# Kernel tuning notes

Measured on AMD Instinct MI355X. Metric: run time of the kernel, lower is better.

Reference implementation:

```python
import jax, jax.numpy as jnp
import numpy as np

B, S, D, H = 4, 2048, 768, 3072

def _layernorm(X):
    # manual LayerNorm: biased variance, no eps, no affine
    mu = jnp.mean(X, axis=2, keepdims=True)
    sigma = jnp.sqrt(jnp.mean(jnp.square(X - mu), axis=2, keepdims=True))
    return (X - mu) / sigma

def setup_inputs() -> dict:
    key = jax.random.key(0)
    ks = jax.random.split(key, 11)
    sc = 0.02
    return {
        "X": jax.random.normal(ks[0], (B, S, D), dtype=jnp.float32),
        "Wq": jax.random.normal(ks[1], (D, D), dtype=jnp.float32) * sc,
        "bq": jnp.zeros((D,), dtype=jnp.float32),
        "Wk": jax.random.normal(ks[2], (D, D), dtype=jnp.float32) * sc,
        "bk": jnp.zeros((D,), dtype=jnp.float32),
        "Wv": jax.random.normal(ks[3], (D, D), dtype=jnp.float32) * sc,
        "bv": jnp.zeros((D,), dtype=jnp.float32),
        "W1": jax.random.normal(ks[4], (D, H), dtype=jnp.float32) * sc,
        "b1": jnp.zeros((H,), dtype=jnp.float32),
        "W2": jax.random.normal(ks[5], (H, D), dtype=jnp.float32) * sc,
        "b2": jnp.zeros((D,), dtype=jnp.float32),
    }

def reference(X, Wq, bq, Wk, bk, Wv, bv, W1, b1, W2, b2):
    dk = jnp.sqrt(jnp.asarray(X.shape[2], dtype=X.dtype))
    Q = X @ Wq + bq
    K = X @ Wk + bk
    V = X @ Wv + bv
    A = jnp.einsum('bqd,bkd->bqk', Q, K)
    # faithful: tril zeroes (not -inf) above-diagonal BEFORE softmax
    A = jnp.tril(A) / dk
    A = jax.nn.softmax(A, axis=2)
    # faithful to einsum 'ijk,ijl->ijl': sum A over k, broadcast onto V
    AV = jnp.sum(A, axis=2, keepdims=True) * V
    X = _layernorm(X + AV)
    F = jax.nn.relu(X @ W1 + b1) @ W2 + b2
    X = _layernorm(X + F)
    return X
```

## Files before the change

kernel.cpp:

```cpp
#include <hip/hip_runtime.h>
#include <hip/hip_bf16.h>
#include <math.h>


typedef __bf16 bf16x8 __attribute__((ext_vector_type(8)));
typedef float f32x4 __attribute__((ext_vector_type(4)));

__device__ inline void gload_lds16(const __hip_bfloat16* g, void* lds) {
  __builtin_amdgcn_global_load_lds(
      (const __attribute__((address_space(1))) void*)g,
      (__attribute__((address_space(3))) void*)lds, 16, 0, 0);
}

__device__ inline float bf2f(unsigned short u) {
  union { unsigned int i; float f; } x;
  x.i = ((unsigned int)u) << 16;
  return x.f;
}

#define BARRIER() asm volatile("s_barrier" ::: "memory")

template <int BNv, int EPI>
__global__ __launch_bounds__(256, 2) void gemm128(
    const __hip_bfloat16* __restrict__ A, const __hip_bfloat16* __restrict__ Bt,
    __hip_bfloat16* __restrict__ C, const float* __restrict__ bias,
    const float* __restrict__ residf, const __hip_bfloat16* __restrict__ residb,
    int M, int N, int K) {
  constexpr int NF = BNv / 32;
  constexpr int BI = BNv / 32;
  constexpr int BS = BNv * 128;
  constexpr int S = 4 + BI;
  __shared__ __align__(16) char smem[32768 + 2 * BS];

  const int bid = blockIdx.x;
  const int mB = M / 128;
  const int rowBase = (bid % mB) * 128;
  const int colBase = (bid / mB) * BNv;
  const int nt = K / 64;

  const int wv = threadIdx.x >> 6;
  const int lane = threadIdx.x & 63;
  const int wr = wv >> 1, wc = wv & 1;
  const int l16 = lane & 15, lk = lane >> 4;

  const int rA = lane >> 3;
  const int cSw = ((lane & 7) ^ rA) * 8;
  const __hip_bfloat16* gA = A + (size_t)(rowBase + wv * 32 + rA) * K + cSw;
  const __hip_bfloat16* gB =
      Bt + (size_t)(colBase + wv * 8 * BI + rA) * K + cSw;

  auto STAGE = [&](int kt, int b) {
    const size_t ko = (size_t)kt * 64;
#pragma unroll
    for (int i = 0; i < 4; ++i)
      gload_lds16(gA + (size_t)i * 8 * K + ko,
                  smem + b * 16384 + (wv * 4 + i) * 1024);
#pragma unroll
    for (int i = 0; i < BI; ++i)
      gload_lds16(gB + (size_t)i * 8 * K + ko,
                  smem + 32768 + b * BS + (wv * BI + i) * 1024);
  };

  const int aBase = (wr * 64 + l16) * 128;
  const int bBase = (wc * (BNv / 2) + l16) * 128;
  const int xr = l16 & 7;
  const int cph0 = ((lk) ^ xr) * 16;
  const int cph1 = ((4 + lk) ^ xr) * 16;

  f32x4 acc[4][NF];
#pragma unroll
  for (int m = 0; m < 4; ++m)
#pragma unroll
    for (int n = 0; n < NF; ++n) acc[m][n] = (f32x4){0.f, 0.f, 0.f, 0.f};

  STAGE(0, 0);
  if (nt > 1) {
    STAGE(1, 1);
    if constexpr (BNv == 128)
      asm volatile("s_waitcnt vmcnt(8)" ::: "memory");
    else
      asm volatile("s_waitcnt vmcnt(7)" ::: "memory");
  } else {
    asm volatile("s_waitcnt vmcnt(0)" ::: "memory");
  }
  BARRIER();

  for (int t = 0; t < nt; ++t) {
    const int b = t & 1;
    const char* pa = smem + b * 16384 + aBase;
    const char* pb = smem + 32768 + b * BS + bBase;

    bf16x8 af0[4], af1[4], bf0[NF], bf1[NF];
#pragma unroll
    for (int m = 0; m < 4; ++m) af0[m] = *(const bf16x8*)(pa + m * 2048 + cph0);
#pragma unroll
    for (int n = 0; n < NF; ++n) bf0[n] = *(const bf16x8*)(pb + n * 2048 + cph0);
#pragma unroll
    for (int m = 0; m < 4; ++m) af1[m] = *(const bf16x8*)(pa + m * 2048 + cph1);
#pragma unroll
    for (int n = 0; n < NF; ++n) bf1[n] = *(const bf16x8*)(pb + n * 2048 + cph1);

    if constexpr (NF == 4)
      asm volatile("s_waitcnt lgkmcnt(8)" ::: "memory");
    else
      asm volatile("s_waitcnt lgkmcnt(7)" ::: "memory");
    __builtin_amdgcn_sched_barrier(0);
    __builtin_amdgcn_s_setprio(1);
#pragma unroll
    for (int m = 0; m < 4; ++m)
#pragma unroll
      for (int n = 0; n < NF; ++n)
        acc[m][n] = __builtin_amdgcn_mfma_f32_16x16x32_bf16(af0[m], bf0[n],
                                                            acc[m][n], 0, 0, 0);
    __builtin_amdgcn_s_setprio(0);
    asm volatile("s_waitcnt lgkmcnt(0)" ::: "memory");
    __builtin_amdgcn_sched_barrier(0);
    __builtin_amdgcn_s_setprio(1);
#pragma unroll
    for (int m = 0; m < 4; ++m)
#pragma unroll
      for (int n = 0; n < NF; ++n)
        acc[m][n] = __builtin_amdgcn_mfma_f32_16x16x32_bf16(af1[m], bf1[n],
                                                            acc[m][n], 0, 0, 0);
    __builtin_amdgcn_s_setprio(0);

    BARRIER();
    if (t + 2 < nt) {
      STAGE(t + 2, b);
      if constexpr (BNv == 128)
        asm volatile("s_waitcnt vmcnt(8)" ::: "memory");
      else
        asm volatile("s_waitcnt vmcnt(7)" ::: "memory");
      BARRIER();
    } else if (t + 2 == nt) {
      asm volatile("s_waitcnt vmcnt(0)" ::: "memory");
      BARRIER();
    }
  }

#pragma unroll
  for (int m = 0; m < 4; ++m) {
#pragma unroll
    for (int n = 0; n < NF; ++n) {
#pragma unroll
      for (int j = 0; j < 4; ++j) {
        const int r = rowBase + wr * 64 + m * 16 + lk * 4 + j;
        const int c = colBase + wc * (BNv / 2) + n * 16 + l16;
        const size_t idx = (size_t)r * N + c;
        float v = acc[m][n][j] + bias[c];
        if (EPI == 1) v += residf[idx];
        if (EPI == 2) v = fmaxf(v, 0.f);
        if (EPI == 3) v += __bfloat162float(residb[idx]);
        C[idx] = __float2bfloat16(v);
      }
    }
  }
}

template <bool OUTF>
__global__ __launch_bounds__(256) void ln_simple(
    const __hip_bfloat16* __restrict__ Y, __hip_bfloat16* __restrict__ outb,
    float* __restrict__ outf) {
  const int wave = threadIdx.x >> 6, lane = threadIdx.x & 63;
  const size_t base = ((size_t)blockIdx.x * 4 + wave) * 768;

  float v[12];
  float s = 0.f, q = 0.f;
#pragma unroll
  for (int c = 0; c < 3; ++c) {
    const int col = c * 256 + lane * 4;
    ushort4 a = *reinterpret_cast<const ushort4*>(&Y[base + col]);
    float y0 = bf2f(a.x), y1 = bf2f(a.y), y2 = bf2f(a.z), y3 = bf2f(a.w);
    v[c * 4 + 0] = y0; v[c * 4 + 1] = y1; v[c * 4 + 2] = y2; v[c * 4 + 3] = y3;
    s += y0 + y1 + y2 + y3;
    q += y0 * y0 + y1 * y1 + y2 * y2 + y3 * y3;
  }
#pragma unroll
  for (int off = 32; off; off >>= 1) {
    s += __shfl_xor(s, off);
    q += __shfl_xor(q, off);
  }
  const float mu = s * (1.f / 768.f);
  const float rs = rsqrtf(q * (1.f / 768.f) - mu * mu);
#pragma unroll
  for (int c = 0; c < 3; ++c) {
    const int col = c * 256 + lane * 4;
    if (OUTF) {
      float4 o;
      o.x = (v[c * 4 + 0] - mu) * rs;
      o.y = (v[c * 4 + 1] - mu) * rs;
      o.z = (v[c * 4 + 2] - mu) * rs;
      o.w = (v[c * 4 + 3] - mu) * rs;
      *reinterpret_cast<float4*>(&outf[base + col]) = o;
    } else {
      __hip_bfloat16 h0 = __float2bfloat16((v[c * 4 + 0] - mu) * rs);
      __hip_bfloat16 h1 = __float2bfloat16((v[c * 4 + 1] - mu) * rs);
      __hip_bfloat16 h2 = __float2bfloat16((v[c * 4 + 2] - mu) * rs);
      __hip_bfloat16 h3 = __float2bfloat16((v[c * 4 + 3] - mu) * rs);
      ushort4 o;
      o.x = *reinterpret_cast<unsigned short*>(&h0);
      o.y = *reinterpret_cast<unsigned short*>(&h1);
      o.z = *reinterpret_cast<unsigned short*>(&h2);
      o.w = *reinterpret_cast<unsigned short*>(&h3);
      *reinterpret_cast<ushort4*>(&outb[base + col]) = o;
    }
  }
}

__global__ __launch_bounds__(256) void cast_bf16_kernel(
    const float* __restrict__ in, __hip_bfloat16* __restrict__ out, int n4) {
  int i = blockIdx.x * blockDim.x + threadIdx.x;
  if (i >= n4) return;
  float4 v = reinterpret_cast<const float4*>(in)[i];
  __hip_bfloat16 h0 = __float2bfloat16(v.x), h1 = __float2bfloat16(v.y);
  __hip_bfloat16 h2 = __float2bfloat16(v.z), h3 = __float2bfloat16(v.w);
  ushort4 o;
  o.x = *reinterpret_cast<unsigned short*>(&h0);
  o.y = *reinterpret_cast<unsigned short*>(&h1);
  o.z = *reinterpret_cast<unsigned short*>(&h2);
  o.w = *reinterpret_cast<unsigned short*>(&h3);
  reinterpret_cast<ushort4*>(out)[i] = o;
}

__global__ __launch_bounds__(256) void transpose_cast(
    const float* __restrict__ W, __hip_bfloat16* __restrict__ Wt, int K, int N) {
  __shared__ float tile[32][33];
  const int t = threadIdx.x;
  const int tx = t & 31;
  const int ty = t >> 5;
  const int n0 = blockIdx.x * 32;
  const int k0 = blockIdx.y * 32;
#pragma unroll
  for (int i = 0; i < 32; i += 8)
    tile[ty + i][tx] = W[(size_t)(k0 + ty + i) * N + n0 + tx];
  __syncthreads();
#pragma unroll
  for (int i = 0; i < 32; i += 8)
    Wt[(size_t)(n0 + ty + i) * K + k0 + tx] = __float2bfloat16(tile[tx][ty + i]);
}

extern "C" void kernel_launch(void* const* d_in, const int* in_sizes, int n_in,
                              void* d_out, int out_size, void* d_ws,
                              size_t ws_size, hipStream_t stream) {
  const float* X = (const float*)d_in[0];
  const float* Wv = (const float*)d_in[5];
  const float* bv = (const float*)d_in[6];
  const float* W1 = (const float*)d_in[7];
  const float* b1 = (const float*)d_in[8];
  const float* W2 = (const float*)d_in[9];
  const float* b2 = (const float*)d_in[10];
  float* out = (float*)d_out;

  const int M = 4 * 2048;
  const int D = 768, H = 3072;

  char* ws = (char*)d_ws;
  __hip_bfloat16* Xb  = (__hip_bfloat16*)(ws);
  __hip_bfloat16* Wvt = (__hip_bfloat16*)(ws + 12582912);
  __hip_bfloat16* W1t = (__hip_bfloat16*)(ws + 13762560);
  __hip_bfloat16* W2t = (__hip_bfloat16*)(ws + 18481152);
  __hip_bfloat16* Yb  = (__hip_bfloat16*)(ws + 23199744);
  __hip_bfloat16* X1b = (__hip_bfloat16*)(ws + 35782656);
  __hip_bfloat16* Gb  = (__hip_bfloat16*)(ws + 48365568);
  __hip_bfloat16* Y2b = Yb;

  cast_bf16_kernel<<<dim3((M * D / 4 + 255) / 256), 256, 0, stream>>>(X, Xb,
                                                                      M * D / 4);
  transpose_cast<<<dim3(D / 32, D / 32), 256, 0, stream>>>(Wv, Wvt, D, D);
  transpose_cast<<<dim3(H / 32, D / 32), 256, 0, stream>>>(W1, W1t, D, H);
  transpose_cast<<<dim3(D / 32, H / 32), 256, 0, stream>>>(W2, W2t, H, D);

  gemm128<96, 1><<<512, 256, 0, stream>>>(Xb, Wvt, Yb, bv, X, nullptr, M, D, D);
  ln_simple<false><<<M / 4, 256, 0, stream>>>(Yb, X1b, nullptr);
  gemm128<128, 2><<<1536, 256, 0, stream>>>(X1b, W1t, Gb, b1, nullptr, nullptr,
                                            M, H, D);
  gemm128<96, 3><<<512, 256, 0, stream>>>(Gb, W2t, Y2b, b2, nullptr, X1b, M, D,
                                          H);
  ln_simple<true><<<M / 4, 256, 0, stream>>>(Y2b, nullptr, out);
}
```

Before: 130.1 us.

## Issue next-stage prefetch mid-iteration and merge prep kernels into one launch

Inside the GEMM main loop, the barrier and the global-to-LDS STAGE load for tile t+2 are moved ahead of the second MFMA half. This lets the prefetch overlap with compute and removes one barrier per iteration. The four preprocessing kernels (X cast and three weight transpose-casts) are merged into a single kernel indexed by block ID, cutting launch overhead. The earlier STAGE may overwrite an LDS buffer while the second MFMA half still reads its fragments; this is only safe if those fragments are already in registers, which the lgkmcnt(0) wait before the barrier appears to ensure.

```diff
diff --git a/kernel.cpp b/kernel.cpp
--- a/kernel.cpp
+++ b/kernel.cpp
@@ -29,7 +29,6 @@
   constexpr int NF = BNv / 32;
   constexpr int BI = BNv / 32;
   constexpr int BS = BNv * 128;
-  constexpr int S = 4 + BI;
   __shared__ __align__(16) char smem[32768 + 2 * BS];
 
   const int bid = blockIdx.x;
@@ -115,6 +114,10 @@
     __builtin_amdgcn_s_setprio(0);
     asm volatile("s_waitcnt lgkmcnt(0)" ::: "memory");
     __builtin_amdgcn_sched_barrier(0);
+    BARRIER();
+
+    if (t + 2 < nt) STAGE(t + 2, b);
+
     __builtin_amdgcn_s_setprio(1);
 #pragma unroll
     for (int m = 0; m < 4; ++m)
@@ -124,16 +127,15 @@
                                                             acc[m][n], 0, 0, 0);
     __builtin_amdgcn_s_setprio(0);
 
-    BARRIER();
-    if (t + 2 < nt) {
-      STAGE(t + 2, b);
-      if constexpr (BNv == 128)
-        asm volatile("s_waitcnt vmcnt(8)" ::: "memory");
-      else
-        asm volatile("s_waitcnt vmcnt(7)" ::: "memory");
-      BARRIER();
-    } else if (t + 2 == nt) {
-      asm volatile("s_waitcnt vmcnt(0)" ::: "memory");
+    if (t + 1 < nt) {
+      if (t + 2 < nt) {
+        if constexpr (BNv == 128)
+          asm volatile("s_waitcnt vmcnt(8)" ::: "memory");
+        else
+          asm volatile("s_waitcnt vmcnt(7)" ::: "memory");
+      } else {
+        asm volatile("s_waitcnt vmcnt(0)" ::: "memory");
+      }
       BARRIER();
     }
   }
@@ -207,29 +209,12 @@
   }
 }
 
-__global__ __launch_bounds__(256) void cast_bf16_kernel(
-    const float* __restrict__ in, __hip_bfloat16* __restrict__ out, int n4) {
-  int i = blockIdx.x * blockDim.x + threadIdx.x;
-  if (i >= n4) return;
-  float4 v = reinterpret_cast<const float4*>(in)[i];
-  __hip_bfloat16 h0 = __float2bfloat16(v.x), h1 = __float2bfloat16(v.y);
-  __hip_bfloat16 h2 = __float2bfloat16(v.z), h3 = __float2bfloat16(v.w);
-  ushort4 o;
-  o.x = *reinterpret_cast<unsigned short*>(&h0);
-  o.y = *reinterpret_cast<unsigned short*>(&h1);
-  o.z = *reinterpret_cast<unsigned short*>(&h2);
-  o.w = *reinterpret_cast<unsigned short*>(&h3);
-  reinterpret_cast<ushort4*>(out)[i] = o;
-}
-
-__global__ __launch_bounds__(256) void transpose_cast(
-    const float* __restrict__ W, __hip_bfloat16* __restrict__ Wt, int K, int N) {
+__device__ inline void tc_tile(const float* __restrict__ W,
+                               __hip_bfloat16* __restrict__ Wt, int K, int N,
+                               int n0, int k0, int t) {
   __shared__ float tile[32][33];
-  const int t = threadIdx.x;
   const int tx = t & 31;
   const int ty = t >> 5;
-  const int n0 = blockIdx.x * 32;
-  const int k0 = blockIdx.y * 32;
 #pragma unroll
   for (int i = 0; i < 32; i += 8)
     tile[ty + i][tx] = W[(size_t)(k0 + ty + i) * N + n0 + tx];
@@ -237,6 +222,36 @@
 #pragma unroll
   for (int i = 0; i < 32; i += 8)
     Wt[(size_t)(n0 + ty + i) * K + k0 + tx] = __float2bfloat16(tile[tx][ty + i]);
+}
+
+__global__ __launch_bounds__(256) void prep_kernel(
+    const float* __restrict__ X, const float* __restrict__ Wv,
+    const float* __restrict__ W1, const float* __restrict__ W2,
+    __hip_bfloat16* __restrict__ Xb, __hip_bfloat16* __restrict__ Wvt,
+    __hip_bfloat16* __restrict__ W1t, __hip_bfloat16* __restrict__ W2t) {
+  const int bid = blockIdx.x;
+  const int t = threadIdx.x;
+  if (bid < 6144) {
+    const int i = bid * 256 + t;
+    float4 v = reinterpret_cast<const float4*>(X)[i];
+    __hip_bfloat16 h0 = __float2bfloat16(v.x), h1 = __float2bfloat16(v.y);
+    __hip_bfloat16 h2 = __float2bfloat16(v.z), h3 = __float2bfloat16(v.w);
+    ushort4 o;
+    o.x = *reinterpret_cast<unsigned short*>(&h0);
+    o.y = *reinterpret_cast<unsigned short*>(&h1);
+    o.z = *reinterpret_cast<unsigned short*>(&h2);
+    o.w = *reinterpret_cast<unsigned short*>(&h3);
+    reinterpret_cast<ushort4*>(Xb)[i] = o;
+  } else if (bid < 6720) {
+    const int idx = bid - 6144;
+    tc_tile(Wv, Wvt, 768, 768, (idx % 24) * 32, (idx / 24) * 32, t);
+  } else if (bid < 9024) {
+    const int idx = bid - 6720;
+    tc_tile(W1, W1t, 768, 3072, (idx % 96) * 32, (idx / 96) * 32, t);
+  } else {
+    const int idx = bid - 9024;
+    tc_tile(W2, W2t, 3072, 768, (idx % 24) * 32, (idx / 24) * 32, t);
+  }
 }
 
 extern "C" void kernel_launch(void* const* d_in, const int* in_sizes, int n_in,
@@ -264,11 +279,7 @@
   __hip_bfloat16* Gb  = (__hip_bfloat16*)(ws + 48365568);
   __hip_bfloat16* Y2b = Yb;
 
-  cast_bf16_kernel<<<dim3((M * D / 4 + 255) / 256), 256, 0, stream>>>(X, Xb,
-                                                                      M * D / 4);
-  transpose_cast<<<dim3(D / 32, D / 32), 256, 0, stream>>>(Wv, Wvt, D, D);
-  transpose_cast<<<dim3(H / 32, D / 32), 256, 0, stream>>>(W1, W1t, D, H);
-  transpose_cast<<<dim3(D / 32, H / 32), 256, 0, stream>>>(W2, W2t, H, D);
+  prep_kernel<<<11328, 256, 0, stream>>>(X, Wv, W1, W2, Xb, Wvt, W1t, W2t);
 
   gemm128<96, 1><<<512, 256, 0, stream>>>(Xb, Wvt, Yb, bv, X, nullptr, M, D, D);
   ln_simple<false><<<M / 4, 256, 0, stream>>>(Yb, X1b, nullptr);
```

New measurement: 125.3 us. 3.7% less time.
